# Optimization experiments

Measured on AMD Instinct MI355X. Metric: run time of the kernel, lower is better.

## Reference

```python
import jax, jax.numpy as jnp
import numpy as np

B, S, HID = 2, 2048, 2048
H, KV, D = 16, 4, 128
ROT = 64           # partial rotary dim (= cos.shape[-1])
EMB = 128          # router embedding dim
TAU, BASE = 0.4, 3.0
EPS = 1e-6


def rotate_half(x):
    h = x.shape[-1] // 2
    return jnp.concatenate([-x[..., h:], x[..., :h]], axis=-1)


def rmsnorm(x, w, eps=EPS):
    # Qwen3.5: zero-init weight, (1 + w) scaling, compute in fp32
    xf = x.astype(jnp.float32)
    o = xf * jax.lax.rsqrt(jnp.mean(xf * xf, axis=-1, keepdims=True) + eps)
    return (o * (1.0 + w.astype(jnp.float32))).astype(x.dtype)


def _rope_tables():
    inv_freq = 1.0 / (10000.0 ** (np.arange(0, ROT, 2, dtype=np.float32) / ROT))
    t = np.arange(S, dtype=np.float32)
    freqs = np.outer(t, inv_freq)                 # [S, ROT/2]
    emb = np.concatenate([freqs, freqs], axis=-1)  # [S, ROT]
    cos = np.broadcast_to(np.cos(emb), (B, S, ROT)).copy()
    sin = np.broadcast_to(np.sin(emb), (B, S, ROT)).copy()
    return jnp.asarray(cos), jnp.asarray(sin)


def setup_inputs() -> dict:
    key = jax.random.key(0)
    ks = jax.random.split(key, 10)
    sc = 0.02
    cos, sin = _rope_tables()
    return {
        "hidden_states": jax.random.normal(ks[0], (B, S, HID), jnp.float32),
        "cos": cos,
        "sin": sin,
        # projection weights stored as [in, out] (torch Linear weight transposed)
        "Wq": jax.random.normal(ks[1], (HID, H * D * 2), jnp.float32) * sc,
        "Wk": jax.random.normal(ks[2], (HID, KV * D), jnp.float32) * sc,
        "Wv": jax.random.normal(ks[3], (HID, KV * D), jnp.float32) * sc,
        "Wo": jax.random.normal(ks[4], (H * D, HID), jnp.float32) * sc,
        "q_norm_w": jnp.zeros((D,), jnp.float32),
        "k_norm_w": jnp.zeros((D,), jnp.float32),
        "Wr": jax.random.normal(ks[5], (HID, EMB), jnp.float32) * sc,   # router linear
        "Wd": jax.random.normal(ks[6], (EMB, D), jnp.float32) * sc,     # router decoder
        "ln_g": jnp.ones((EMB,), jnp.float32),
        "ln_b": jnp.zeros((EMB,), jnp.float32),
        "rnn_state": jnp.zeros((EMB,), jnp.float32),
    }


def _forward(hidden_states, cos, sin, Wq, Wk, Wv, Wo, q_norm_w, k_norm_w,
             Wr, Wd, ln_g, ln_b, rnn_state):
    b, s, _ = hidden_states.shape
    # doubled q_proj -> query + gate
    qkv = jnp.einsum('bsh,hd->bsd', hidden_states, Wq).reshape(b, s, H, 2 * D)
    q, gate = qkv[..., :D], qkv[..., D:]
    gate = gate.reshape(b, s, H * D)
    k = jnp.einsum('bsh,hd->bsd', hidden_states, Wk).reshape(b, s, KV, D)
    v = jnp.einsum('bsh,hd->bsd', hidden_states, Wv).reshape(b, s, KV, D)
    # per-head RMSNorm then [b, h, s, d]
    q = rmsnorm(q, q_norm_w).transpose(0, 2, 1, 3)
    k = rmsnorm(k, k_norm_w).transpose(0, 2, 1, 3)
    v = v.transpose(0, 2, 1, 3)

    # --- head-dim router (gumbel-sigmoid, straight-through hard round) ---
    emb = jnp.einsum('bsh,he->bse', hidden_states, Wr) + rnn_state
    mu = jnp.mean(emb, -1, keepdims=True)
    var = jnp.mean((emb - mu) ** 2, -1, keepdims=True)
    ln = (emb - mu) * jax.lax.rsqrt(var + 1e-5) * ln_g + ln_b
    logits = jnp.einsum('bse,ed->bsd', jax.nn.gelu(ln, approximate=False), Wd)
    gum = -jnp.log(jax.random.exponential(jax.random.key(42), logits.shape, jnp.float32))
    y_soft = jax.nn.sigmoid((logits + gum + BASE) / TAU)
    binary = jax.lax.stop_gradient(jnp.round(y_soft) - y_soft) + y_soft  # [b, s, D]
    mask = binary[:, None, :, :]  # broadcast over heads: [b, 1, s, D]

    q = q * mask
    k = k * mask

    # partial RoPE on first ROT dims (qk_index=None training path)
    c = cos[:, None, :, :]
    si = sin[:, None, :, :]
    def rope(x):
        xr, xp = x[..., :ROT], x[..., ROT:]
        return jnp.concatenate([xr * c + rotate_half(xr) * si, xp], axis=-1)
    q = rope(q)
    k = rope(k)

    # GQA: repeat kv heads
    rep = H // KV
    k = jnp.repeat(k, rep, axis=1)
    v = jnp.repeat(v, rep, axis=1)

    scores = jnp.einsum('bhqd,bhkd->bhqk', q, k) / np.sqrt(D).astype(np.float32)
    causal = jnp.tril(jnp.ones((s, s), bool))
    scores = jnp.where(causal, scores, jnp.finfo(jnp.float32).min)
    attn = jax.nn.softmax(scores.astype(jnp.float32), axis=-1).astype(q.dtype)
    out = jnp.einsum('bhqk,bhkd->bhqd', attn, v)
    out = out.transpose(0, 2, 1, 3).reshape(b, s, H * D)
    out = out * jax.nn.sigmoid(gate)   # output gate
    return jnp.einsum('bsd,dh->bsh', out, Wo)


def reference(hidden_states, cos, sin, Wq, Wk, Wv, Wo, q_norm_w, k_norm_w,
              Wr, Wd, ln_g, ln_b, rnn_state):
    return _forward(hidden_states, cos, sin, Wq, Wk, Wv, Wo, q_norm_w, k_norm_w,
                    Wr, Wd, ln_g, ln_b, rnn_state)
```

## Files before the change

### kernel.cpp

```cpp
#include <hip/hip_runtime.h>
#include <math.h>

typedef __bf16 bf16;
typedef bf16 bf16x8 __attribute__((ext_vector_type(8)));
typedef bf16 bf16x4 __attribute__((ext_vector_type(4)));
typedef float f32x4 __attribute__((ext_vector_type(4)));

#define BB 2
#define SS 2048
#define NPROJ 5248
#define QSCALE (0.08838834764831845f * 1.4426950408889634f)
#define USHIFT 32.0f

__device__ __forceinline__ float waveAllReduceSum(float v) {
#pragma unroll
  for (int o = 1; o < 64; o <<= 1) v += __shfl_xor(v, o, 64);
  return v;
}

__device__ __forceinline__ int xcd_swz(int orig, int nwg) {
  return (orig & 7) * (nwg >> 3) + (orig >> 3);
}

__device__ __forceinline__ void gload16(const bf16* g, bf16* l) {
  __builtin_amdgcn_global_load_lds((const __attribute__((address_space(1))) void*)g,
                                   (__attribute__((address_space(3))) void*)l, 16, 0, 0);
}

__device__ __forceinline__ void do_transpose(bf16 (*tile)[72], const float* __restrict__ W,
                                             bf16* __restrict__ WT, int K, int N, int rowOff,
                                             int bx, int by, int t) {
  int n0 = bx * 64, k0 = by * 64;
  {
    int c4 = (t & 15) * 4, r = t >> 4;
#pragma unroll
    for (int p = 0; p < 4; p++) {
      int row = p * 16 + r;
      float4 v = *reinterpret_cast<const float4*>(W + (size_t)(k0 + row) * N + n0 + c4);
      bf16x4 o = {(bf16)v.x, (bf16)v.y, (bf16)v.z, (bf16)v.w};
      *reinterpret_cast<bf16x4*>(&tile[row][c4]) = o;
    }
  }
  __syncthreads();
  {
    int ln = t & 7, n = t >> 3;
#pragma unroll
    for (int p = 0; p < 2; p++) {
      int nn = p * 32 + n;
      bf16x8 o;
#pragma unroll
      for (int j = 0; j < 8; j++) o[j] = tile[ln * 8 + j][nn];
      *reinterpret_cast<bf16x8*>(WT + (size_t)(rowOff + n0 + nn) * K + k0 + ln * 8) = o;
    }
  }
  __syncthreads();
}

__global__ __launch_bounds__(256) void prep_weights(const float* __restrict__ hidden,
                                                    const float* __restrict__ Wq,
                                                    const float* __restrict__ Wk,
                                                    const float* __restrict__ Wv,
                                                    const float* __restrict__ Wr,
                                                    const float* __restrict__ Wo,
                                                    bf16* __restrict__ hb,
                                                    bf16* __restrict__ WTall,
                                                    bf16* __restrict__ WoT) {
  __shared__ bf16 tile[64][72];
  int id = blockIdx.x, t = threadIdx.x;
  if (id < 4096) {
    int i = (id * 256 + t) * 8;
    float4 v0 = *reinterpret_cast<const float4*>(hidden + i);
    float4 v1 = *reinterpret_cast<const float4*>(hidden + i + 4);
    bf16x8 o = {(bf16)v0.x, (bf16)v0.y, (bf16)v0.z, (bf16)v0.w,
                (bf16)v1.x, (bf16)v1.y, (bf16)v1.z, (bf16)v1.w};
    *reinterpret_cast<bf16x8*>(hb + i) = o;
    return;
  }
  int id2 = id - 4096;
  if (id2 < 2048) { do_transpose(tile, Wq, WTall, 2048, 4096, 0, id2 & 63, id2 >> 6, t); return; }
  id2 -= 2048;
  if (id2 < 256) { do_transpose(tile, Wk, WTall, 2048, 512, 4096, id2 & 7, id2 >> 3, t); return; }
  id2 -= 256;
  if (id2 < 256) { do_transpose(tile, Wv, WTall, 2048, 512, 4608, id2 & 7, id2 >> 3, t); return; }
  id2 -= 256;
  if (id2 < 64) { do_transpose(tile, Wr, WTall, 2048, 128, 5120, id2 & 1, id2 >> 1, t); return; }
  id2 -= 64;
  do_transpose(tile, Wo, WoT, 2048, 2048, 0, id2 & 31, id2 >> 5, t);
}

template <typename CT>
__global__ __launch_bounds__(256) void gemm_bt(const bf16* __restrict__ A,
                                               const bf16* __restrict__ Bt,
                                               CT* __restrict__ C, int M, int N, int K) {
  __shared__ bf16 lA[128 * 64];
  __shared__ bf16 lB[128 * 64];
  const int nbx = N >> 7;
  int wg = xcd_swz(blockIdx.x, gridDim.x);
  int bx = wg % nbx, by = wg / nbx;
  const int t = threadIdx.x;
  const int l = t & 63, w = t >> 6;
  const int wr = w >> 1, wc = w & 1;
  const int lr = l & 15, lhi = l >> 4;

  f32x4 acc[4][4];
#pragma unroll
  for (int m = 0; m < 4; m++)
#pragma unroll
    for (int n = 0; n < 4; n++) acc[m][n] = f32x4{0.f, 0.f, 0.f, 0.f};

  const int rowA0 = by * 128, rowB0 = bx * 128;
  const int nkt = K >> 6;
  for (int kt = 0; kt < nkt; ++kt) {
    __syncthreads();
#pragma unroll
    for (int it = 0; it < 4; ++it) {
      int slot = it * 256 + t;
      int row = slot >> 3, sl = slot & 7;
      gload16(A + (size_t)(rowA0 + row) * K + kt * 64 + ((sl ^ (row & 7)) << 3), lA + slot * 8);
      gload16(Bt + (size_t)(rowB0 + row) * K + kt * 64 + ((sl ^ (row & 7)) << 3), lB + slot * 8);
    }
    __syncthreads();
#pragma unroll
    for (int kc = 0; kc < 2; ++kc) {
      bf16x8 af[4], bg[4];
#pragma unroll
      for (int m = 0; m < 4; m++) {
        int row = wr * 64 + m * 16 + lr;
        af[m] = *reinterpret_cast<const bf16x8*>((char*)lA + row * 128 + (((kc * 4 + lhi) ^ (row & 7)) << 4));
      }
#pragma unroll
      for (int n = 0; n < 4; n++) {
        int row = wc * 64 + n * 16 + lr;
        bg[n] = *reinterpret_cast<const bf16x8*>((char*)lB + row * 128 + (((kc * 4 + lhi) ^ (row & 7)) << 4));
      }
      __builtin_amdgcn_s_setprio(1);
#pragma unroll
      for (int m = 0; m < 4; m++)
#pragma unroll
        for (int n = 0; n < 4; n++)
          acc[m][n] = __builtin_amdgcn_mfma_f32_16x16x32_bf16(af[m], bg[n], acc[m][n], 0, 0, 0);
      __builtin_amdgcn_s_setprio(0);
    }
  }
#pragma unroll
  for (int m = 0; m < 4; m++)
#pragma unroll
    for (int n = 0; n < 4; n++)
#pragma unroll
      for (int r = 0; r < 4; r++) {
        int grow = rowA0 + wr * 64 + m * 16 + lhi * 4 + r;
        int gcol = rowB0 + wc * 64 + n * 16 + lr;
        C[(size_t)grow * N + gcol] = (CT)acc[m][n][r];
      }
}

__device__ __forceinline__ unsigned rotl32(unsigned x, int r) { return (x << r) | (x >> (32 - r)); }

__device__ __forceinline__ float gumbel42(unsigned i) {
  const unsigned half = (unsigned)(BB * SS * 128) / 2u;
  unsigned x0, x1;
  int word;
  if (i < half) { x0 = i; x1 = i + half; word = 0; }
  else          { x0 = i - half; x1 = i; word = 1; }
  const unsigned k0 = 0u, k1 = 42u;
  const unsigned k2 = k0 ^ k1 ^ 0x1BD11BDAu;
  x0 += k0; x1 += k1;
#define TF_R(r) { x0 += x1; x1 = rotl32(x1, r); x1 ^= x0; }
  TF_R(13) TF_R(15) TF_R(26) TF_R(6)
  x0 += k1; x1 += k2 + 1u;
  TF_R(17) TF_R(29) TF_R(16) TF_R(24)
  x0 += k2; x1 += k0 + 2u;
  TF_R(13) TF_R(15) TF_R(26) TF_R(6)
  x0 += k0; x1 += k1 + 3u;
  TF_R(17) TF_R(29) TF_R(16) TF_R(24)
  x0 += k1; x1 += k2 + 4u;
  TF_R(13) TF_R(15) TF_R(26) TF_R(6)
  x0 += k2; x1 += k0 + 5u;
#undef TF_R
  unsigned bits = word ? x1 : x0;
  float u = __uint_as_float((bits >> 9) | 0x3f800000u) - 1.0f;
  float ex = -log1pf(-u);
  return -logf(ex);
}

__global__ __launch_bounds__(128) void mask_kernel(const bf16* __restrict__ qkva,
                                                   const float* __restrict__ rnn,
                                                   const float* __restrict__ lng,
                                                   const float* __restrict__ lnb,
                                                   const float* __restrict__ Wd,
                                                   bf16* __restrict__ maskb) {
  int row = blockIdx.x;
  int t = threadIdx.x;
  int l = t & 63, w = t >> 6;
  __shared__ float redm[2], redv[2], gsh[128];
  float e = (float)qkva[(size_t)row * NPROJ + 5120 + t] + rnn[t];
  float s1 = waveAllReduceSum(e);
  if (l == 0) redm[w] = s1;
  __syncthreads();
  float mu = (redm[0] + redm[1]) * (1.0f / 128.0f);
  float dv = (e - mu) * (e - mu);
  float s2 = waveAllReduceSum(dv);
  if (l == 0) redv[w] = s2;
  __syncthreads();
  float var = (redv[0] + redv[1]) * (1.0f / 128.0f);
  float ln = (e - mu) * rsqrtf(var + 1e-5f) * lng[t] + lnb[t];
  float g = 0.5f * ln * (1.0f + erff(ln * 0.7071067811865475f));
  gsh[t] = g;
  __syncthreads();
  float logit = 0.f;
#pragma unroll 8
  for (int e2 = 0; e2 < 128; e2++) logit += gsh[e2] * Wd[e2 * 128 + t];
  float gum = gumbel42((unsigned)(row * 128 + t));
  float x = (logit + gum + 3.0f) * 2.5f;
  float y = 1.0f / (1.0f + expf(-x));
  maskb[(size_t)row * 128 + t] = (bf16)rintf(y);
}

__global__ __launch_bounds__(256) void qkv_prep(const bf16* __restrict__ qkva,
                                                const bf16* __restrict__ maskb,
                                                const float* __restrict__ qw,
                                                const float* __restrict__ kw,
                                                const float* __restrict__ cosT,
                                                const float* __restrict__ sinT,
                                                bf16* __restrict__ wq,
                                                bf16* __restrict__ sgate,
                                                bf16* __restrict__ wk,
                                                bf16* __restrict__ wvt) {
  int id = blockIdx.x, t = threadIdx.x;
  if (id < 4096) {
    int g = t >> 4, ln = t & 15;
    int hr = id * 16 + g;
    int h = hr & 15, row = hr >> 4;
    int b = row >> 11, s = row & 2047;
    const bf16* qp = qkva + (size_t)row * NPROJ + h * 256 + ln * 8;
    bf16x8 q8 = *reinterpret_cast<const bf16x8*>(qp);
    bf16x8 g8 = *reinterpret_cast<const bf16x8*>(qp + 128);
    bf16x8 m8 = *reinterpret_cast<const bf16x8*>(maskb + (size_t)row * 128 + ln * 8);
    float qf[8], ss = 0.f;
#pragma unroll
    for (int j = 0; j < 8; j++) { qf[j] = (float)q8[j]; ss += qf[j] * qf[j]; }
#pragma unroll
    for (int o = 1; o < 16; o <<= 1) ss += __shfl_xor(ss, o, 16);
    float rinv = rsqrtf(ss * (1.0f / 128.0f) + 1e-6f);
    alignas(16) float wv[8];
    const float4* qw4 = reinterpret_cast<const float4*>(qw);
    *reinterpret_cast<float4*>(&wv[0]) = qw4[ln * 2];
    *reinterpret_cast<float4*>(&wv[4]) = qw4[ln * 2 + 1];
    float qm[8];
#pragma unroll
    for (int j = 0; j < 8; j++) qm[j] = qf[j] * rinv * (1.0f + wv[j]) * (float)m8[j];
    alignas(16) float c8[8], s8[8];
    if (ln < 8) {
      const float4* c4 = reinterpret_cast<const float4*>(cosT + (size_t)row * 64);
      const float4* sn4 = reinterpret_cast<const float4*>(sinT + (size_t)row * 64);
      *reinterpret_cast<float4*>(&c8[0]) = c4[ln * 2];
      *reinterpret_cast<float4*>(&c8[4]) = c4[ln * 2 + 1];
      *reinterpret_cast<float4*>(&s8[0]) = sn4[ln * 2];
      *reinterpret_cast<float4*>(&s8[4]) = sn4[ln * 2 + 1];
    }
    float po[8];
#pragma unroll
    for (int j = 0; j < 8; j++) po[j] = __shfl_xor(qm[j], 4, 16);
    bf16x8 oq, og;
#pragma unroll
    for (int j = 0; j < 8; j++) {
      float ov;
      if (ln < 4) ov = qm[j] * c8[j] - po[j] * s8[j];
      else if (ln < 8) ov = qm[j] * c8[j] + po[j] * s8[j];
      else ov = qm[j];
      oq[j] = (bf16)(ov * QSCALE);
      og[j] = (bf16)(1.0f / (1.0f + expf(-(float)g8[j])));
    }
    size_t o = ((size_t)((b * 16 + h) * 2048 + s)) * 128 + ln * 8;
    *reinterpret_cast<bf16x8*>(wq + o) = oq;
    *reinterpret_cast<bf16x8*>(sgate + o) = og;
    return;
  }
  if (id < 5120) {
    int g = t >> 4, ln = t & 15;
    int hr = (id - 4096) * 16 + g;
    int kv = hr & 3, row = hr >> 2;
    int b = row >> 11, s = row & 2047;
    const bf16* kp = qkva + (size_t)row * NPROJ + 4096 + kv * 128 + ln * 8;
    bf16x8 k8 = *reinterpret_cast<const bf16x8*>(kp);
    bf16x8 m8 = *reinterpret_cast<const bf16x8*>(maskb + (size_t)row * 128 + ln * 8);
    float kf[8], ss = 0.f;
#pragma unroll
    for (int j = 0; j < 8; j++) { kf[j] = (float)k8[j]; ss += kf[j] * kf[j]; }
#pragma unroll
    for (int o = 1; o < 16; o <<= 1) ss += __shfl_xor(ss, o, 16);
    float rinv = rsqrtf(ss * (1.0f / 128.0f) + 1e-6f);
    alignas(16) float wv[8];
    const float4* kw4 = reinterpret_cast<const float4*>(kw);
    *reinterpret_cast<float4*>(&wv[0]) = kw4[ln * 2];
    *reinterpret_cast<float4*>(&wv[4]) = kw4[ln * 2 + 1];
    float km[8];
#pragma unroll
    for (int j = 0; j < 8; j++) km[j] = kf[j] * rinv * (1.0f + wv[j]) * (float)m8[j];
    alignas(16) float c8[8], s8[8];
    if (ln < 8) {
      const float4* c4 = reinterpret_cast<const float4*>(cosT + (size_t)row * 64);
      const float4* sn4 = reinterpret_cast<const float4*>(sinT + (size_t)row * 64);
      *reinterpret_cast<float4*>(&c8[0]) = c4[ln * 2];
      *reinterpret_cast<float4*>(&c8[4]) = c4[ln * 2 + 1];
      *reinterpret_cast<float4*>(&s8[0]) = sn4[ln * 2];
      *reinterpret_cast<float4*>(&s8[4]) = sn4[ln * 2 + 1];
    }
    float po[8];
#pragma unroll
    for (int j = 0; j < 8; j++) po[j] = __shfl_xor(km[j], 4, 16);
    bf16x8 ok;
#pragma unroll
    for (int j = 0; j < 8; j++) {
      float ov;
      if (ln < 4) ov = km[j] * c8[j] - po[j] * s8[j];
      else if (ln < 8) ov = km[j] * c8[j] + po[j] * s8[j];
      else ov = km[j];
      ok[j] = (bf16)ov;
    }
    *reinterpret_cast<bf16x8*>(wk + ((size_t)((b * 4 + kv) * 2048 + s)) * 128 + ln * 8) = ok;
    return;
  }
  {
    __shared__ bf16 tl[64][72];
    int vb = id - 5120;
    int dt = vb & 1;
    int st = (vb >> 1) & 31;
    int bkv = vb >> 6;
    int b = bkv >> 2, kv = bkv & 3;
    int tx = t & 63, ty = t >> 6;
    int s0 = st * 64, d0 = dt * 64;
#pragma unroll
    for (int i = 0; i < 16; i++) {
      int srow = ty + i * 4;
      tl[srow][tx] = qkva[(size_t)(b * 2048 + s0 + srow) * NPROJ + 4608 + kv * 128 + d0 + tx];
    }
    __syncthreads();
#pragma unroll
    for (int i = 0; i < 16; i++) {
      int drow = ty + i * 4;
      wvt[(size_t)((b * 4 + kv) * 128 + d0 + drow) * 2048 + s0 + tx] = tl[tx][drow];
    }
  }
}

__global__ __launch_bounds__(512) void attn_kernel(const bf16* __restrict__ wq,
                                                   const bf16* __restrict__ wk,
                                                   const bf16* __restrict__ wvt,
                                                   const bf16* __restrict__ sgate,
                                                   bf16* __restrict__ wattn) {
  __shared__ bf16 lK[2][64 * 128];
  __shared__ bf16 lV[2][128 * 64];
  __shared__ bf16 lP[8][16 * 64];
  int bid = blockIdx.x;
  int grp = bid & 7;
  int b = grp >> 2, kvh = grp & 3;
  int g32 = bid >> 3;
  int pp = g32 & 7;
  int h = kvh * 4 + (g32 >> 3);
  int bh = b * 16 + h;
  int t = threadIdx.x, l = t & 63, w = t >> 6;
  int lr = l & 15, lhi = l >> 4;

  const bf16* kbase = wk + (size_t)((b * 4 + kvh) * 2048) * 128;
  const bf16* vbase = wvt + (size_t)((b * 4 + kvh) * 128) * 2048;
  char* pb = (char*)(&lP[w][0]);

  const int n0 = 2 * pp + 2;

  auto stage = [&](int buf, int tt) {
#pragma unroll
    for (int it = 0; it < 2; ++it) {
      int slot = it * 512 + t;
      int row = slot >> 4, sl = slot & 15;
      gload16(kbase + (size_t)(tt * 64 + row) * 128 + ((sl ^ (row & 7)) << 3), lK[buf] + slot * 8);
      int row2 = slot >> 3, sl2 = slot & 7;
      gload16(vbase + (size_t)row2 * 2048 + tt * 64 + ((sl2 ^ (row2 & 7)) << 3), lV[buf] + slot * 8);
    }
  };

  bf16x8 aq[4];
  f32x4 oacc[8];
  float l_run;
  int qb128 = pp;

  auto load_q = [&](int qbv) {
    const bf16* qbase = wq + (size_t)(bh * 2048 + qbv * 128 + w * 16) * 128;
#pragma unroll
    for (int kc = 0; kc < 4; kc++)
      aq[kc] = *reinterpret_cast<const bf16x8*>(qbase + (size_t)lr * 128 + kc * 32 + lhi * 8);
  };
  load_q(pp);
#pragma unroll
  for (int db = 0; db < 8; db++) oacc[db] = f32x4{0.f, 0.f, 0.f, 0.f};
  l_run = 0.f;

  stage(0, 0);
  __syncthreads();
  int cur = 0;

  for (int i = 0; i < 34; ++i) {
    int tt = (i < n0) ? i : i - n0;
    if (i + 1 < 34) {
      int tn = (i + 1 < n0) ? (i + 1) : (i + 1 - n0);
      stage(cur ^ 1, tn);
    }
    int qrow0 = qb128 * 128 + w * 16;

    f32x4 sacc[4];
#pragma unroll
    for (int j = 0; j < 4; j++) sacc[j] = f32x4{0.f, 0.f, 0.f, 0.f};
    __builtin_amdgcn_s_setprio(1);
#pragma unroll
    for (int kc = 0; kc < 4; kc++)
#pragma unroll
      for (int j = 0; j < 4; j++) {
        int row = j * 16 + lr;
        bf16x8 ak = *reinterpret_cast<const bf16x8*>((char*)lK[cur] + row * 256 + (((kc * 4 + lhi) ^ (row & 7)) << 4));
        sacc[j] = __builtin_amdgcn_mfma_f32_16x16x32_bf16(ak, aq[kc], sacc[j], 0, 0, 0);
      }
    __builtin_amdgcn_s_setprio(0);

    if (tt * 64 + 63 > qrow0) {
      int qrow_g = qrow0 + lr;
#pragma unroll
      for (int j = 0; j < 4; j++)
#pragma unroll
        for (int r = 0; r < 4; r++) {
          int kg = tt * 64 + j * 16 + lhi * 4 + r;
          if (kg > qrow_g) sacc[j][r] = -1e30f;
        }
    }

    float p[4][4];
    float rs = 0.f;
#pragma unroll
    for (int j = 0; j < 4; j++) {
#pragma unroll
      for (int r = 0; r < 4; r++) {
        float pv = exp2f(sacc[j][r] - USHIFT);
        p[j][r] = pv;
        rs += pv;
      }
    }
    l_run += rs;

#pragma unroll
    for (int j = 0; j < 4; j++) {
      bf16x4 p4 = {(bf16)p[j][0], (bf16)p[j][1], (bf16)p[j][2], (bf16)p[j][3]};
      *reinterpret_cast<bf16x4*>(pb + lr * 128 + ((j * 32 + lhi * 8) ^ ((lr & 7) << 4))) = p4;
    }
    bf16x8 pa[2];
#pragma unroll
    for (int kc2 = 0; kc2 < 2; kc2++)
      pa[kc2] = *reinterpret_cast<const bf16x8*>(pb + lr * 128 + ((kc2 * 64 + lhi * 16) ^ ((lr & 7) << 4)));
    __builtin_amdgcn_s_setprio(1);
#pragma unroll
    for (int kc2 = 0; kc2 < 2; kc2++)
#pragma unroll
      for (int db = 0; db < 8; db++) {
        int row = db * 16 + lr;
        bf16x8 bv = *reinterpret_cast<const bf16x8*>((char*)lV[cur] + row * 128 + (((kc2 * 4 + lhi) ^ (row & 7)) << 4));
        oacc[db] = __builtin_amdgcn_mfma_f32_16x16x32_bf16(pa[kc2], bv, oacc[db], 0, 0, 0);
      }
    __builtin_amdgcn_s_setprio(0);

    if (i == n0 - 1 || i == 33) {
      float lsum = l_run;
      lsum += __shfl_xor(lsum, 16, 64);
      lsum += __shfl_xor(lsum, 32, 64);
      float linv[4];
#pragma unroll
      for (int r = 0; r < 4; r++) linv[r] = 1.0f / __shfl(lsum, lhi * 4 + r, 64);
#pragma unroll
      for (int r = 0; r < 4; r++) {
        int srow = qb128 * 128 + w * 16 + lhi * 4 + r;
#pragma unroll
        for (int db = 0; db < 8; db++) {
          int dcol = db * 16 + lr;
          float g = (float)sgate[(size_t)(bh * 2048 + srow) * 128 + dcol];
          float ov = oacc[db][r] * linv[r] * g;
          wattn[(size_t)(b * 2048 + srow) * 2048 + h * 128 + dcol] = (bf16)ov;
        }
      }
      if (i == n0 - 1) {
        qb128 = 15 - pp;
        load_q(qb128);
#pragma unroll
        for (int db = 0; db < 8; db++) oacc[db] = f32x4{0.f, 0.f, 0.f, 0.f};
        l_run = 0.f;
      }
    }

    __syncthreads();
    cur ^= 1;
  }
}

extern "C" void kernel_launch(void* const* d_in, const int* in_sizes, int n_in,
                              void* d_out, int out_size, void* d_ws, size_t ws_size,
                              hipStream_t stream) {
  const float* hidden = (const float*)d_in[0];
  const float* cosT = (const float*)d_in[1];
  const float* sinT = (const float*)d_in[2];
  const float* Wq = (const float*)d_in[3];
  const float* Wk = (const float*)d_in[4];
  const float* Wv = (const float*)d_in[5];
  const float* Wo = (const float*)d_in[6];
  const float* qw = (const float*)d_in[7];
  const float* kw = (const float*)d_in[8];
  const float* Wr = (const float*)d_in[9];
  const float* Wd = (const float*)d_in[10];
  const float* lng = (const float*)d_in[11];
  const float* lnb = (const float*)d_in[12];
  const float* rnn = (const float*)d_in[13];
  float* out = (float*)d_out;

  char* p = (char*)d_ws;
  auto alloc = [&](size_t bytes) { char* r = p; p += (bytes + 255) & ~(size_t)255; return r; };
  bf16* hb    = (bf16*)alloc((size_t)4096 * 2048 * 2);
  bf16* WTall = (bf16*)alloc((size_t)NPROJ * 2048 * 2);
  bf16* WoT   = (bf16*)alloc((size_t)2048 * 2048 * 2);
  bf16* qkva  = (bf16*)alloc((size_t)4096 * NPROJ * 2);
  bf16* maskb = (bf16*)alloc((size_t)4096 * 128 * 2);
  bf16* wqb   = (bf16*)alloc((size_t)2 * 16 * 2048 * 128 * 2);
  bf16* wkb   = (bf16*)alloc((size_t)2 * 4 * 2048 * 128 * 2);
  bf16* wvtb  = (bf16*)alloc((size_t)2 * 4 * 128 * 2048 * 2);
  bf16* sgb   = (bf16*)alloc((size_t)2 * 16 * 2048 * 128 * 2);
  bf16* wab   = (bf16*)alloc((size_t)4096 * 2048 * 2);
  if ((size_t)(p - (char*)d_ws) > ws_size) return;

  prep_weights<<<7744, 256, 0, stream>>>(hidden, Wq, Wk, Wv, Wr, Wo, hb, WTall, WoT);

  gemm_bt<bf16><<<41 * 32, 256, 0, stream>>>(hb, WTall, qkva, 4096, NPROJ, 2048);

  mask_kernel<<<4096, 128, 0, stream>>>(qkva, rnn, lng, lnb, Wd, maskb);
  qkv_prep<<<5632, 256, 0, stream>>>(qkva, maskb, qw, kw, cosT, sinT, wqb, sgb, wkb, wvtb);

  attn_kernel<<<256, 512, 0, stream>>>(wqb, wkb, wvtb, sgb, wab);

  gemm_bt<float><<<16 * 32, 256, 0, stream>>>(wab, WoT, out, 4096, 2048, 2048);
}
```

Baseline: 271.4 us.

## Fuse Q RMSNorm/RoPE/mask and sigmoid gate into attention kernel

```diff
diff --git a/kernel.cpp b/kernel.cpp
--- a/kernel.cpp
+++ b/kernel.cpp
@@ -218,67 +218,15 @@
 
 __global__ __launch_bounds__(256) void qkv_prep(const bf16* __restrict__ qkva,
                                                 const bf16* __restrict__ maskb,
-                                                const float* __restrict__ qw,
                                                 const float* __restrict__ kw,
                                                 const float* __restrict__ cosT,
                                                 const float* __restrict__ sinT,
-                                                bf16* __restrict__ wq,
-                                                bf16* __restrict__ sgate,
                                                 bf16* __restrict__ wk,
                                                 bf16* __restrict__ wvt) {
   int id = blockIdx.x, t = threadIdx.x;
-  if (id < 4096) {
+  if (id < 1024) {
     int g = t >> 4, ln = t & 15;
     int hr = id * 16 + g;
-    int h = hr & 15, row = hr >> 4;
-    int b = row >> 11, s = row & 2047;
-    const bf16* qp = qkva + (size_t)row * NPROJ + h * 256 + ln * 8;
-    bf16x8 q8 = *reinterpret_cast<const bf16x8*>(qp);
-    bf16x8 g8 = *reinterpret_cast<const bf16x8*>(qp + 128);
-    bf16x8 m8 = *reinterpret_cast<const bf16x8*>(maskb + (size_t)row * 128 + ln * 8);
-    float qf[8], ss = 0.f;
-#pragma unroll
-    for (int j = 0; j < 8; j++) { qf[j] = (float)q8[j]; ss += qf[j] * qf[j]; }
-#pragma unroll
-    for (int o = 1; o < 16; o <<= 1) ss += __shfl_xor(ss, o, 16);
-    float rinv = rsqrtf(ss * (1.0f / 128.0f) + 1e-6f);
-    alignas(16) float wv[8];
-    const float4* qw4 = reinterpret_cast<const float4*>(qw);
-    *reinterpret_cast<float4*>(&wv[0]) = qw4[ln * 2];
-    *reinterpret_cast<float4*>(&wv[4]) = qw4[ln * 2 + 1];
-    float qm[8];
-#pragma unroll
-    for (int j = 0; j < 8; j++) qm[j] = qf[j] * rinv * (1.0f + wv[j]) * (float)m8[j];
-    alignas(16) float c8[8], s8[8];
-    if (ln < 8) {
-      const float4* c4 = reinterpret_cast<const float4*>(cosT + (size_t)row * 64);
-      const float4* sn4 = reinterpret_cast<const float4*>(sinT + (size_t)row * 64);
-      *reinterpret_cast<float4*>(&c8[0]) = c4[ln * 2];
-      *reinterpret_cast<float4*>(&c8[4]) = c4[ln * 2 + 1];
-      *reinterpret_cast<float4*>(&s8[0]) = sn4[ln * 2];
-      *reinterpret_cast<float4*>(&s8[4]) = sn4[ln * 2 + 1];
-    }
-    float po[8];
-#pragma unroll
-    for (int j = 0; j < 8; j++) po[j] = __shfl_xor(qm[j], 4, 16);
-    bf16x8 oq, og;
-#pragma unroll
-    for (int j = 0; j < 8; j++) {
-      float ov;
-      if (ln < 4) ov = qm[j] * c8[j] - po[j] * s8[j];
-      else if (ln < 8) ov = qm[j] * c8[j] + po[j] * s8[j];
-      else ov = qm[j];
-      oq[j] = (bf16)(ov * QSCALE);
-      og[j] = (bf16)(1.0f / (1.0f + expf(-(float)g8[j])));
-    }
-    size_t o = ((size_t)((b * 16 + h) * 2048 + s)) * 128 + ln * 8;
-    *reinterpret_cast<bf16x8*>(wq + o) = oq;
-    *reinterpret_cast<bf16x8*>(sgate + o) = og;
-    return;
-  }
-  if (id < 5120) {
-    int g = t >> 4, ln = t & 15;
-    int hr = (id - 4096) * 16 + g;
     int kv = hr & 3, row = hr >> 2;
     int b = row >> 11, s = row & 2047;
     const bf16* kp = qkva + (size_t)row * NPROJ + 4096 + kv * 128 + ln * 8;
@@ -323,7 +271,7 @@
   }
   {
     __shared__ bf16 tl[64][72];
-    int vb = id - 5120;
+    int vb = id - 1024;
     int dt = vb & 1;
     int st = (vb >> 1) & 31;
     int bkv = vb >> 6;
@@ -344,10 +292,13 @@
   }
 }
 
-__global__ __launch_bounds__(512) void attn_kernel(const bf16* __restrict__ wq,
+__global__ __launch_bounds__(512) void attn_kernel(const bf16* __restrict__ qkva,
                                                    const bf16* __restrict__ wk,
                                                    const bf16* __restrict__ wvt,
-                                                   const bf16* __restrict__ sgate,
+                                                   const bf16* __restrict__ maskb,
+                                                   const float* __restrict__ qw,
+                                                   const float* __restrict__ cosT,
+                                                   const float* __restrict__ sinT,
                                                    bf16* __restrict__ wattn) {
   __shared__ bf16 lK[2][64 * 128];
   __shared__ bf16 lV[2][128 * 64];
@@ -385,11 +336,56 @@
   int qb128 = pp;
 
   auto load_q = [&](int qbv) {
-    const bf16* qbase = wq + (size_t)(bh * 2048 + qbv * 128 + w * 16) * 128;
-#pragma unroll
-    for (int kc = 0; kc < 4; kc++)
-      aq[kc] = *reinterpret_cast<const bf16x8*>(qbase + (size_t)lr * 128 + kc * 32 + lhi * 8);
+    int srow = qbv * 128 + w * 16 + lr;
+    int grow = b * 2048 + srow;
+    const bf16* qp = qkva + (size_t)grow * NPROJ + h * 256;
+    int dbase = lhi * 8;
+    float qf[4][8];
+    float ss = 0.f;
+#pragma unroll
+    for (int kc = 0; kc < 4; kc++) {
+      bf16x8 v = *reinterpret_cast<const bf16x8*>(qp + kc * 32 + dbase);
+#pragma unroll
+      for (int j = 0; j < 8; j++) { qf[kc][j] = (float)v[j]; ss += qf[kc][j] * qf[kc][j]; }
+    }
+    ss += __shfl_xor(ss, 16, 64);
+    ss += __shfl_xor(ss, 32, 64);
+    float rinv = rsqrtf(ss * (1.0f / 128.0f) + 1e-6f);
+    const bf16* mrow = maskb + (size_t)grow * 128;
+    float qm[4][8];
+#pragma unroll
+    for (int kc = 0; kc < 4; kc++) {
+      bf16x8 m8 = *reinterpret_cast<const bf16x8*>(mrow + kc * 32 + dbase);
+      float4 wa = *reinterpret_cast<const float4*>(qw + kc * 32 + dbase);
+      float4 wb = *reinterpret_cast<const float4*>(qw + kc * 32 + dbase + 4);
+      alignas(16) float wv[8];
+      *reinterpret_cast<float4*>(&wv[0]) = wa;
+      *reinterpret_cast<float4*>(&wv[4]) = wb;
+#pragma unroll
+      for (int j = 0; j < 8; j++) qm[kc][j] = qf[kc][j] * rinv * (1.0f + wv[j]) * (float)m8[j];
+    }
+    const float* crow = cosT + (size_t)grow * 64;
+    const float* srw = sinT + (size_t)grow * 64;
+    alignas(16) float c0[8], c1[8], s0[8], s1[8];
+    *reinterpret_cast<float4*>(&c0[0]) = *reinterpret_cast<const float4*>(crow + dbase);
+    *reinterpret_cast<float4*>(&c0[4]) = *reinterpret_cast<const float4*>(crow + dbase + 4);
+    *reinterpret_cast<float4*>(&c1[0]) = *reinterpret_cast<const float4*>(crow + 32 + dbase);
+    *reinterpret_cast<float4*>(&c1[4]) = *reinterpret_cast<const float4*>(crow + 32 + dbase + 4);
+    *reinterpret_cast<float4*>(&s0[0]) = *reinterpret_cast<const float4*>(srw + dbase);
+    *reinterpret_cast<float4*>(&s0[4]) = *reinterpret_cast<const float4*>(srw + dbase + 4);
+    *reinterpret_cast<float4*>(&s1[0]) = *reinterpret_cast<const float4*>(srw + 32 + dbase);
+    *reinterpret_cast<float4*>(&s1[4]) = *reinterpret_cast<const float4*>(srw + 32 + dbase + 4);
+#pragma unroll
+    for (int j = 0; j < 8; j++) {
+      float o0 = qm[0][j] * c0[j] - qm[1][j] * s0[j];
+      float o1 = qm[1][j] * c1[j] + qm[0][j] * s1[j];
+      aq[0][j] = (bf16)(o0 * QSCALE);
+      aq[1][j] = (bf16)(o1 * QSCALE);
+      aq[2][j] = (bf16)(qm[2][j] * QSCALE);
+      aq[3][j] = (bf16)(qm[3][j] * QSCALE);
+    }
   };
+
   load_q(pp);
 #pragma unroll
   for (int db = 0; db < 8; db++) oacc[db] = f32x4{0.f, 0.f, 0.f, 0.f};
@@ -475,10 +471,12 @@
 #pragma unroll
       for (int r = 0; r < 4; r++) {
         int srow = qb128 * 128 + w * 16 + lhi * 4 + r;
+        const bf16* grow_p = qkva + (size_t)(b * 2048 + srow) * NPROJ + h * 256 + 128;
 #pragma unroll
         for (int db = 0; db < 8; db++) {
           int dcol = db * 16 + lr;
-          float g = (float)sgate[(size_t)(bh * 2048 + srow) * 128 + dcol];
+          float graw = (float)grow_p[dcol];
+          float g = 1.0f / (1.0f + expf(-graw));
           float ov = oacc[db][r] * linv[r] * g;
           wattn[(size_t)(b * 2048 + srow) * 2048 + h * 128 + dcol] = (bf16)ov;
         }
@@ -523,10 +521,8 @@
   bf16* WoT   = (bf16*)alloc((size_t)2048 * 2048 * 2);
   bf16* qkva  = (bf16*)alloc((size_t)4096 * NPROJ * 2);
   bf16* maskb = (bf16*)alloc((size_t)4096 * 128 * 2);
-  bf16* wqb   = (bf16*)alloc((size_t)2 * 16 * 2048 * 128 * 2);
   bf16* wkb   = (bf16*)alloc((size_t)2 * 4 * 2048 * 128 * 2);
   bf16* wvtb  = (bf16*)alloc((size_t)2 * 4 * 128 * 2048 * 2);
-  bf16* sgb   = (bf16*)alloc((size_t)2 * 16 * 2048 * 128 * 2);
   bf16* wab   = (bf16*)alloc((size_t)4096 * 2048 * 2);
   if ((size_t)(p - (char*)d_ws) > ws_size) return;
 
@@ -535,9 +531,9 @@
   gemm_bt<bf16><<<41 * 32, 256, 0, stream>>>(hb, WTall, qkva, 4096, NPROJ, 2048);
 
   mask_kernel<<<4096, 128, 0, stream>>>(qkva, rnn, lng, lnb, Wd, maskb);
-  qkv_prep<<<5632, 256, 0, stream>>>(qkva, maskb, qw, kw, cosT, sinT, wqb, sgb, wkb, wvtb);
-
-  attn_kernel<<<256, 512, 0, stream>>>(wqb, wkb, wvtb, sgb, wab);
+  qkv_prep<<<1536, 256, 0, stream>>>(qkva, maskb, kw, cosT, sinT, wkb, wvtb);
+
+  attn_kernel<<<256, 512, 0, stream>>>(qkva, wkb, wvtb, maskb, qw, cosT, sinT, wab);
 
   gemm_bt<float><<<16 * 32, 256, 0, stream>>>(wab, WoT, out, 4096, 2048, 2048);
 }
```

Result: no change. 268.5 us (-1.1%).
